# Kernel tuning notes

Hardware: AMD Instinct MI355X
Metric: run time of the kernel (lower is better)

The kernel has to match this reference:

```python
import jax, jax.numpy as jnp
import numpy as np

B, S, N = 16, 64, 4096
D = 64            # input_dim*seq_len == output_dim*graph_dim
FEAT = 64
E = 32768
HEADS = (3, 3, 1)
NEG_SLOPE = 0.2   # PyG GATConv default negative_slope


def _lin_init(key, fi, fo):
    k1, k2 = jax.random.split(key)
    s = 1.0 / np.sqrt(fi)
    return (jax.random.uniform(k1, (fi, fo), jnp.float32, -s, s),
            jax.random.uniform(k2, (fo,), jnp.float32, -s, s))


def setup_inputs() -> dict:
    key = jax.random.key(0)
    ks = jax.random.split(key, 32)
    inp = {}
    inp["inputs"] = jax.random.normal(ks[0], (B, S, N, 1), jnp.float32)
    inp["edge_index"] = jax.random.randint(ks[1], (2, E), 0, N, dtype=jnp.int32)
    inp["W_seq"], inp["b_seq"] = _lin_init(ks[2], D, D)
    inp["src_embed"] = jax.random.normal(ks[3], (N, FEAT), jnp.float32) * 0.1
    inp["tgt_embed"] = jax.random.normal(ks[4], (FEAT, N), jnp.float32) * 0.1
    for i, H in enumerate(HEADS):
        s = 1.0 / np.sqrt(D)
        inp[f"Wg{i}"] = jax.random.uniform(ks[5 + 5 * i], (D, H * D), jnp.float32, -s, s)
        inp[f"asrc{i}"] = jax.random.normal(ks[6 + 5 * i], (H, D), jnp.float32) * 0.1
        inp[f"adst{i}"] = jax.random.normal(ks[7 + 5 * i], (H, D), jnp.float32) * 0.1
        inp[f"bg{i}"] = jnp.zeros((D,), jnp.float32)
        inp[f"Wl{i}"], inp[f"bl{i}"] = _lin_init(ks[8 + 5 * i], D, D)
    inp["Wo"], inp["bo"] = _lin_init(ks[25], D, D)
    return inp


def _gat(x, src, dst, W, a_src, a_dst, b):
    # PyG GATConv, concat=False (mean over heads). x: [B,N,D] -> [B,N,D]
    H, C = a_src.shape
    xp = jnp.einsum('bnd,dhc->bnhc', x, W.reshape(D, H, C))       # [B,N,H,C]
    al_s = jnp.einsum('bnhc,hc->bnh', xp, a_src)
    al_d = jnp.einsum('bnhc,hc->bnh', xp, a_dst)
    e = jax.nn.leaky_relu(al_s[:, src] + al_d[:, dst], NEG_SLOPE)  # [B,Et,H]

    def per_graph(e_b, xj_b):
        m = jax.ops.segment_max(e_b, dst, num_segments=N)          # [N,H]
        w = jnp.exp(e_b - m[dst])
        z = jax.ops.segment_sum(w, dst, num_segments=N)
        alpha = w / z[dst]                                         # softmax per dst node
        return jax.ops.segment_sum(xj_b * alpha[..., None], dst, num_segments=N)

    out = jax.vmap(per_graph)(e, xp[:, src])                       # [B,N,H,C]
    return out.mean(axis=2) + b


def _forward(inputs, edge_index, W_seq, b_seq, src_embed, tgt_embed,
             Wg0, asrc0, adst0, bg0, Wl0, bl0,
             Wg1, asrc1, adst1, bg1, Wl1, bl1,
             Wg2, asrc2, adst2, bg2, Wl2, bl2, Wo, bo):
    loop = jnp.arange(N, dtype=edge_index.dtype)
    src = jnp.concatenate([edge_index[0], loop])   # PyG add_self_loops=True
    dst = jnp.concatenate([edge_index[1], loop])
    h = inputs.transpose(0, 2, 3, 1).reshape(B * N, D)
    h = h @ W_seq + b_seq + h                       # seq_linear residual
    A = jax.nn.softmax(jax.nn.relu(src_embed @ tgt_embed), axis=1)  # learned adjacency [N,N]
    gat_p = [(Wg0, asrc0, adst0, bg0), (Wg1, asrc1, adst1, bg1), (Wg2, asrc2, adst2, bg2)]
    lin_p = [(Wl0, bl0), (Wl1, bl1), (Wl2, bl2)]
    for i in range(3):
        hb = h.reshape(B, N, D)
        # layer-0 GAT output is computed but unused in the original code (dead); skip it
        h_cur = _gat(hb, src, dst, *gat_p[i]).reshape(B * N, D) if i > 0 else None
        adp = jnp.einsum('mn,bnd->bmd', A, hb)      # adaptive-graph matmul (dropout in eval = identity)
        adp = (adp @ lin_p[i][0] + lin_p[i][1]).reshape(B * N, D)
        g = jax.nn.sigmoid(adp)
        if i == 0:
            origin = h @ Wo + bo
            h = jnp.tanh(h) * g + origin * (1.0 - g)
        elif i == 1:
            h = jax.nn.leaky_relu(h_cur, 0.01) * g + h * (1.0 - g)
        else:
            h = jax.nn.relu(h_cur) * g + h * (1.0 - g)
    return h.reshape(B, N, 1, D)   # [batch, node_num, output_dim, graph_dim]


def reference(inputs, edge_index, W_seq, b_seq, src_embed, tgt_embed,
              Wg0, asrc0, adst0, bg0, Wl0, bl0,
              Wg1, asrc1, adst1, bg1, Wl1, bl1,
              Wg2, asrc2, adst2, bg2, Wl2, bl2, Wo, bo):
    return _forward(inputs, edge_index, W_seq, b_seq, src_embed, tgt_embed,
                    Wg0, asrc0, adst0, bg0, Wl0, bl0,
                    Wg1, asrc1, adst1, bg1, Wl1, bl1,
                    Wg2, asrc2, adst2, bg2, Wl2, bl2, Wo, bo)
```

## Files before the change

kernel.cpp:

```cpp
#include <hip/hip_runtime.h>
#include <stdint.h>

#define NB 16
#define NN 4096
#define DD 64
#define EE 32768
#define ETOT 36864
#define ROWS 65536
#define KSPLIT 4

typedef _Float16 f16;
typedef f16   half8 __attribute__((ext_vector_type(8)));
typedef f16   f16x8 __attribute__((ext_vector_type(8)));
typedef f16   f16x4 __attribute__((ext_vector_type(4)));
typedef float f32x4 __attribute__((ext_vector_type(4)));

__device__ __forceinline__ void gload16(const f16* g, f16* l) {
  __builtin_amdgcn_global_load_lds((const __attribute__((address_space(1))) void*)g,
                                   (__attribute__((address_space(3))) void*)l, 16, 0, 0);
}

__global__ __launch_bounds__(256) void k_zero2(int* a, int* b) {
  int i = blockIdx.x * 256 + threadIdx.x;
  if (i < NN) a[i] = 0;
  else if (i < 2 * NN) b[i - NN] = 0;
}

__global__ __launch_bounds__(256) void k_count(const int* __restrict__ ei, int* __restrict__ cnt) {
  int t = blockIdx.x * 256 + threadIdx.x;
  if (t >= ETOT) return;
  int d = (t < EE) ? ei[EE + t] : (t - EE);
  atomicAdd(&cnt[d], 1);
}

__global__ __launch_bounds__(256) void k_scan(const int* __restrict__ cnt, int* __restrict__ offs) {
  __shared__ int part[256];
  int t = threadIdx.x;
  int loc[16]; int s = 0;
  #pragma unroll
  for (int i = 0; i < 16; ++i) { int v = cnt[(t << 4) + i]; loc[i] = s; s += v; }
  part[t] = s;
  __syncthreads();
  int own = s;
  for (int d = 1; d < 256; d <<= 1) {
    int u = (t >= d) ? part[t - d] : 0;
    __syncthreads();
    part[t] += u;
    __syncthreads();
  }
  int base = part[t] - own;
  #pragma unroll
  for (int i = 0; i < 16; ++i) offs[(t << 4) + i] = base + loc[i];
}

__global__ __launch_bounds__(256) void k_fill(const int* __restrict__ ei, const int* __restrict__ offs,
                                              int* __restrict__ cur, int* __restrict__ esrc) {
  int t = blockIdx.x * 256 + threadIdx.x;
  if (t >= ETOT) return;
  int s, d;
  if (t < EE) { s = ei[t]; d = ei[EE + t]; } else { s = d = t - EE; }
  int p = atomicAdd(&cur[d], 1);
  esrc[offs[d] + p] = s;
}

__global__ __launch_bounds__(256) void k_seq(const float* __restrict__ inp, const float* __restrict__ Wseq,
                                             const float* __restrict__ bseq, float* __restrict__ h) {
  __shared__ float X[64 * 68];
  int t = threadIdx.x;
  int b = blockIdx.x >> 6, n0 = (blockIdx.x & 63) << 6;
  #pragma unroll
  for (int i = 0; i < 16; ++i) {
    int idx = t + (i << 8);
    int s = idx >> 6, nl = idx & 63;
    X[nl * 68 + s] = inp[((size_t)((b << 6) + s) << 12) + n0 + nl];
  }
  __syncthreads();
  int c = t & 63, rg = t >> 6;
  float Wc[64];
  #pragma unroll
  for (int k = 0; k < 64; ++k) Wc[k] = Wseq[(k << 6) + c];
  float bc = bseq[c];
  for (int rr = 0; rr < 16; ++rr) {
    int r = (rg << 4) + rr;
    float a = bc + X[r * 68 + c];
    #pragma unroll
    for (int k4 = 0; k4 < 16; ++k4) {
      float4 x = *(const float4*)&X[r * 68 + (k4 << 2)];
      a = fmaf(x.x, Wc[4*k4+0], a); a = fmaf(x.y, Wc[4*k4+1], a);
      a = fmaf(x.z, Wc[4*k4+2], a); a = fmaf(x.w, Wc[4*k4+3], a);
    }
    h[((size_t)(b << 12) + n0 + r) * 64 + c] = a;
  }
}

__global__ __launch_bounds__(256) void k_adjmm(const f16* __restrict__ SEh, const f16* __restrict__ TEh,
                                               f16* __restrict__ A, float* __restrict__ Zpart) {
  __shared__ f16 Al[2][128 * 32];
  __shared__ f16 Bl[2][128 * 32];
  const int t = threadIdx.x, lane = t & 63, w = t >> 6;
  const int m0 = blockIdx.y << 7, j0 = blockIdx.x << 7;
  const int l15 = lane & 15, lhi = lane >> 4;
  const int wm = (w >> 1) << 6, wj = (w & 1) << 6;
  f32x4 acc[4][4] = {};
  const int c0 = (w << 6) + lane;
  const int row0 = c0 >> 2, ko0 = (c0 & 3) << 3;
  const int c1 = c0 + 256;
  const int row1 = c1 >> 2, ko1 = (c1 & 3) << 3;
  const f16* ga0 = SEh + (size_t)(m0 + row0) * 64 + ko0;
  const f16* ga1 = SEh + (size_t)(m0 + row1) * 64 + ko1;
  const f16* gb0 = TEh + (size_t)(j0 + row0) * 64 + ko0;
  const f16* gb1 = TEh + (size_t)(j0 + row1) * 64 + ko1;
  #pragma unroll
  for (int kt = 0; kt < 2; ++kt) {
    const int kof = kt << 5;
    gload16(ga0 + kof, Al[kt] + c0 * 8);
    gload16(ga1 + kof, Al[kt] + c1 * 8);
    gload16(gb0 + kof, Bl[kt] + c0 * 8);
    gload16(gb1 + kof, Bl[kt] + c1 * 8);
  }
  __syncthreads();
  #pragma unroll
  for (int kt = 0; kt < 2; ++kt) {
    half8 af[4], bf[4];
    #pragma unroll
    for (int i = 0; i < 4; ++i) {
      af[i] = *(const half8*)(Al[kt] + (wm + i * 16 + l15) * 32 + lhi * 8);
      bf[i] = *(const half8*)(Bl[kt] + (wj + i * 16 + l15) * 32 + lhi * 8);
    }
    #pragma unroll
    for (int mi = 0; mi < 4; ++mi)
      #pragma unroll
      for (int nj = 0; nj < 4; ++nj)
        acc[mi][nj] = __builtin_amdgcn_mfma_f32_16x16x32_f16(af[mi], bf[nj], acc[mi][nj], 0, 0, 0);
  }
  float rs[4][4];
  #pragma unroll
  for (int mi = 0; mi < 4; ++mi)
    #pragma unroll
    for (int r = 0; r < 4; ++r) rs[mi][r] = 0.f;
  #pragma unroll
  for (int mi = 0; mi < 4; ++mi)
    #pragma unroll
    for (int nj = 0; nj < 4; ++nj)
      #pragma unroll
      for (int r = 0; r < 4; ++r) {
        int row = m0 + wm + mi * 16 + lhi * 4 + r;
        int col = j0 + wj + nj * 16 + l15;
        float e = __expf(fmaxf(acc[mi][nj][r], 0.f));
        f16 eh = (f16)e;
        A[((size_t)row << 12) + col] = eh;
        rs[mi][r] += (float)eh;
      }
  #pragma unroll
  for (int mi = 0; mi < 4; ++mi)
    #pragma unroll
    for (int r = 0; r < 4; ++r) {
      float s = rs[mi][r];
      s += __shfl_xor(s, 1); s += __shfl_xor(s, 2);
      s += __shfl_xor(s, 4); s += __shfl_xor(s, 8);
      rs[mi][r] = s;
    }
  if (l15 == 0) {
    int p = (blockIdx.x << 1) + (w & 1);
    #pragma unroll
    for (int mi = 0; mi < 4; ++mi)
      #pragma unroll
      for (int r = 0; r < 4; ++r)
        Zpart[((size_t)p << 12) + m0 + wm + mi * 16 + lhi * 4 + r] = rs[mi][r];
  }
}

__global__ __launch_bounds__(256) void k_rowz(const float* __restrict__ Zpart, float* __restrict__ rowZ) {
  int row = blockIdx.x * 256 + threadIdx.x;
  float s = 0.f;
  #pragma unroll 8
  for (int p = 0; p < 64; ++p) s += Zpart[((size_t)p << 12) + row];
  rowZ[row] = 1.f / s;
}

#define NKT 16
__global__ __launch_bounds__(512) void k_gemm8(const f16* __restrict__ A, const f16* __restrict__ BT,
                                               f16* __restrict__ Cout) {
  extern __shared__ f16 smem[];
  const int t = threadIdx.x, lane = t & 63, wid = t >> 6;
  const int wr = wid >> 2, wc = wid & 3;
  const int l15 = lane & 15, lhi = lane >> 4;
  const int h7 = l15 & 7;
  const int wgid = blockIdx.x;
  const int nid = (wgid & 7) * 32 + (wgid >> 3);
  const int z = nid >> 6, rem = nid & 63;
  const int m0 = (rem >> 2) << 8;
  const int j0 = (rem & 3) << 8;
  const size_t kbase = (size_t)z << 10;
  f16* __restrict__ Cz = Cout + ((size_t)z << 22);

  const f16* gA[4]; int lA[4];
  #pragma unroll
  for (int i = 0; i < 4; ++i) {
    int s = t + (i << 9), row = s >> 3, sl = (s & 7) ^ (row & 7);
    gA[i] = A + (size_t)(m0 + row) * 4096 + kbase + sl * 8;
    lA[i] = s * 8;
  }
  const f16* gB[4]; int lB[4];
  #pragma unroll
  for (int i = 0; i < 4; ++i) {
    int s = t + (i << 9), row = s >> 3, sl = (s & 7) ^ (row & 7);
    gB[i] = BT + (size_t)(j0 + row) * 4096 + kbase + sl * 8;
    lB[i] = 16384 + s * 8;
  }
  #define SA(buf, kt, i) gload16(gA[i] + (kt) * 64, smem + (buf) * 32768 + lA[i])
  #define SB(buf, kt, i) gload16(gB[i] + (kt) * 64, smem + (buf) * 32768 + lB[i])

  const int rbase = wr << 7;
  const int cbase = wc << 6;
  f32x4 acc[8][4] = {};

  #pragma unroll
  for (int i = 0; i < 4; ++i) SA(0, 0, i);
  #pragma unroll
  for (int i = 0; i < 4; ++i) SB(0, 0, i);
  asm volatile("s_waitcnt vmcnt(0)" ::: "memory");
  __builtin_amdgcn_sched_barrier(0);
  __builtin_amdgcn_s_barrier();
  __builtin_amdgcn_sched_barrier(0);

  for (int kt = 0; kt < NKT; ++kt) {
    const int cur = kt & 1;
    const f16* Ab = smem + cur * 32768;
    const f16* Bb = Ab + 16384;
    const bool pf = (kt + 1 < NKT);
    {
      half8 af[8], bf[4];
      #pragma unroll
      for (int mi = 0; mi < 8; ++mi) {
        int row = rbase + mi * 16 + l15;
        af[mi] = *(const half8*)(Ab + row * 64 + (lhi ^ h7) * 8);
      }
      #pragma unroll
      for (int nj = 0; nj < 4; ++nj) {
        int row = cbase + nj * 16 + l15;
        bf[nj] = *(const half8*)(Bb + row * 64 + (lhi ^ h7) * 8);
      }
      if (pf) { SA(cur ^ 1, kt + 1, 0); SA(cur ^ 1, kt + 1, 1); SA(cur ^ 1, kt + 1, 2); SA(cur ^ 1, kt + 1, 3); }
      __builtin_amdgcn_s_setprio(1);
      #pragma unroll
      for (int mi = 0; mi < 8; ++mi)
        #pragma unroll
        for (int nj = 0; nj < 4; ++nj)
          acc[mi][nj] = __builtin_amdgcn_mfma_f32_16x16x32_f16(af[mi], bf[nj], acc[mi][nj], 0, 0, 0);
      __builtin_amdgcn_s_setprio(0);
    }
    {
      half8 af[8], bf[4];
      #pragma unroll
      for (int mi = 0; mi < 8; ++mi) {
        int row = rbase + mi * 16 + l15;
        af[mi] = *(const half8*)(Ab + row * 64 + ((4 + lhi) ^ h7) * 8);
      }
      #pragma unroll
      for (int nj = 0; nj < 4; ++nj) {
        int row = cbase + nj * 16 + l15;
        bf[nj] = *(const half8*)(Bb + row * 64 + ((4 + lhi) ^ h7) * 8);
      }
      if (pf) { SB(cur ^ 1, kt + 1, 0); SB(cur ^ 1, kt + 1, 1); SB(cur ^ 1, kt + 1, 2); SB(cur ^ 1, kt + 1, 3); }
      __builtin_amdgcn_s_setprio(1);
      #pragma unroll
      for (int mi = 0; mi < 8; ++mi)
        #pragma unroll
        for (int nj = 0; nj < 4; ++nj)
          acc[mi][nj] = __builtin_amdgcn_mfma_f32_16x16x32_f16(af[mi], bf[nj], acc[mi][nj], 0, 0, 0);
      __builtin_amdgcn_s_setprio(0);
    }
    if (pf) {
      asm volatile("s_waitcnt vmcnt(0)" ::: "memory");
      __builtin_amdgcn_sched_barrier(0);
      __builtin_amdgcn_s_barrier();
      __builtin_amdgcn_sched_barrier(0);
    }
  }
  #undef SA
  #undef SB
  #pragma unroll
  for (int mi = 0; mi < 8; ++mi)
    #pragma unroll
    for (int nj = 0; nj < 4; ++nj)
      #pragma unroll
      for (int r = 0; r < 4; ++r) {
        int row = m0 + rbase + mi * 16 + (lhi << 2) + r;
        int col = j0 + cbase + nj * 16 + l15;
        Cz[(size_t)row * 1024 + col] = (f16)acc[mi][nj][r];
      }
}

template<int H, int NP>
__device__ __forceinline__ void wprep_body(const float* __restrict__ Wg, const float* __restrict__ asrc,
                                           const float* __restrict__ adst, const float* __restrict__ Wl,
                                           f16* __restrict__ Wgh, int bid, int t) {
  const int WL0 = H * 64 + 16;
  for (int i = bid * 256 + t; i < NP * 64; i += 16 * 256) {
    int j = i >> 6, k = i & 63;
    float v;
    if (j < H * 64) {
      v = Wg[(size_t)k * (H * 64) + j];
    } else if (j < H * 64 + 2 * H) {
      int cc = j - H * 64, hh = cc >> 1;
      const float* a = ((cc & 1) ? adst : asrc) + (hh << 6);
      const float* wrow = Wg + (size_t)k * (H * 64) + (hh << 6);
      float s = 0.f;
      #pragma unroll 16
      for (int c = 0; c < 64; ++c) s = fmaf(wrow[c], a[c], s);
      v = s;
    } else if (j >= WL0 && j < WL0 + 64) {
      v = Wl[(k << 6) + (j - WL0)];
    } else v = 0.f;
    Wgh[(size_t)j * 64 + k] = (f16)v;
  }
}

__global__ __launch_bounds__(256) void k_allprep(
    const float* __restrict__ Wg1, const float* __restrict__ as1, const float* __restrict__ ad1,
    const float* __restrict__ Wl1, f16* __restrict__ Wgh1,
    const float* __restrict__ Wg2, const float* __restrict__ as2, const float* __restrict__ ad2,
    const float* __restrict__ Wl2, f16* __restrict__ Wgh2,
    const float* __restrict__ Wl0, const float* __restrict__ Wo, f16* __restrict__ W0h,
    const float* __restrict__ SE, const float* __restrict__ TE,
    f16* __restrict__ SEh, f16* __restrict__ TEh) {
  __shared__ float X[64 * 65];
  int bid = blockIdx.x, t = threadIdx.x;
  if (bid < 16) { wprep_body<3, 272>(Wg1, as1, ad1, Wl1, Wgh1, bid, t); return; }
  if (bid < 32) { wprep_body<1, 144>(Wg2, as2, ad2, Wl2, Wgh2, bid - 16, t); return; }
  if (bid < 40) {
    for (int i = (bid - 32) * 256 + t; i < 128 * 64; i += 8 * 256) {
      int j = i >> 6, k = i & 63;
      float v = (j < 64) ? Wl0[(k << 6) + j] : Wo[(k << 6) + (j - 64)];
      W0h[(size_t)j * 64 + k] = (f16)v;
    }
    return;
  }
  if (bid < 296) {
    int i = ((bid - 40) * 256 + t) * 4;
    float4 v = *(const float4*)(SE + i);
    f16 o[4] = {(f16)v.x, (f16)v.y, (f16)v.z, (f16)v.w};
    *(uint64_t*)(SEh + i) = *(uint64_t*)o;
    return;
  }
  int j0 = (bid - 296) << 6;
  #pragma unroll
  for (int i = 0; i < 16; ++i) {
    int idx = t + (i << 8);
    int k = idx >> 6, jl = idx & 63;
    X[jl * 65 + k] = TE[((size_t)k << 12) + j0 + jl];
  }
  __syncthreads();
  int jl = t >> 2, kg = t & 3;
  f16 o[16];
  #pragma unroll
  for (int i = 0; i < 16; ++i) o[i] = (f16)X[jl * 65 + (kg << 4) + i];
  f16* dst = TEh + ((size_t)(j0 + jl) << 6) + (kg << 4);
  *(uint64_t*)(dst + 0) = *(uint64_t*)(o + 0);
  *(uint64_t*)(dst + 4) = *(uint64_t*)(o + 4);
  *(uint64_t*)(dst + 8) = *(uint64_t*)(o + 8);
  *(uint64_t*)(dst + 12) = *(uint64_t*)(o + 12);
}

template<int H, int NP>
__global__ __launch_bounds__(256) void k_xpmm(const float* __restrict__ h, const f16* __restrict__ Wgh,
                                              f16* __restrict__ xp, float* __restrict__ als4,
                                              float* __restrict__ ald4, f16* __restrict__ HWlT) {
  const int WL0 = H * 64 + 16, JW0 = WL0 / 16, NT = NP / 16;
  __shared__ f16 Ah[64 * 72];
  __shared__ f16 Bh[NP * 72];
  __shared__ f16 stage[64 * 72];
  const int t = threadIdx.x, lane = t & 63, w = t >> 6;
  const size_t r0 = (size_t)blockIdx.x * 64;
  const int b = (int)(r0 >> 12), n0 = (int)(r0 & 4095);
  #pragma unroll
  for (int i = 0; i < 4; ++i) {
    int idx = t + (i << 8);
    int row = idx >> 4, k4 = (idx & 15) << 2;
    float4 v = *(const float4*)&h[(r0 + row) * 64 + k4];
    f16 o[4] = {(f16)v.x, (f16)v.y, (f16)v.z, (f16)v.w};
    *(uint64_t*)&Ah[row * 72 + k4] = *(uint64_t*)o;
  }
  for (int i = t; i < NP * 16; i += 256) {
    int row = i >> 4, k4 = (i & 15) << 2;
    *(uint64_t*)&Bh[row * 72 + k4] = *(const uint64_t*)&Wgh[(size_t)row * 64 + k4];
  }
  __syncthreads();
  const int l15 = lane & 15, lhi = lane >> 4;
  f32x4 acc[NT] = {};
  #pragma unroll
  for (int kk = 0; kk < 2; ++kk) {
    half8 af = *(const half8*)&Ah[(w * 16 + l15) * 72 + kk * 32 + lhi * 8];
    #pragma unroll
    for (int j = 0; j < NT; ++j) {
      half8 bf = *(const half8*)&Bh[(j * 16 + l15) * 72 + kk * 32 + lhi * 8];
      acc[j] = __builtin_amdgcn_mfma_f32_16x16x32_f16(af, bf, acc[j], 0, 0, 0);
    }
  }
  const int rl = w * 16 + lhi * 4;
  #pragma unroll
  for (int j = 0; j < NT; ++j) {
    int col = j * 16 + l15;
    if (j * 16 + 15 < H * 64) {
      #pragma unroll
      for (int r = 0; r < 4; ++r) {
        if (H == 3) xp[(r0 + rl + r) * 256 + ((col & 63) << 2) + (col >> 6)] = (f16)acc[j][r];
        else        xp[(r0 + rl + r) * 64 + col] = (f16)acc[j][r];
      }
    } else if (j < JW0) {
      int cc = col - H * 64;
      if (cc >= 0 && cc < 2 * H) {
        int hh = cc >> 1;
        #pragma unroll
        for (int r = 0; r < 4; ++r) {
          if (cc & 1) ald4[(r0 + rl + r) * 4 + hh] = acc[j][r];
          else        als4[(r0 + rl + r) * 4 + hh] = acc[j][r];
        }
      }
    } else {
      int e = col - WL0;
      f16 o[4] = {(f16)acc[j][0], (f16)acc[j][1], (f16)acc[j][2], (f16)acc[j][3]};
      *(uint64_t*)&stage[e * 72 + rl] = *(uint64_t*)o;
    }
  }
  __syncthreads();
  {
    int e = t >> 2, seg = (t & 3) << 4;
    float4 v0 = *(const float4*)&stage[e * 72 + seg];
    float4 v1 = *(const float4*)&stage[e * 72 + seg + 8];
    f16* dst = HWlT + (((size_t)((b << 6) + e)) << 12) + n0 + seg;
    *(float4*)dst = v0;
    *(float4*)(dst + 8) = v1;
  }
}

__global__ __launch_bounds__(256) void k_prep0(const float* __restrict__ h, const f16* __restrict__ W0h,
                                               f16* __restrict__ HWlT, f16* __restrict__ orig) {
  __shared__ f16 Ah[64 * 72];
  __shared__ f16 Bh[128 * 72];
  __shared__ f16 stage[64 * 72];
  const int t = threadIdx.x, lane = t & 63, w = t >> 6;
  const size_t r0 = (size_t)blockIdx.x * 64;
  const int b = (int)(r0 >> 12), n0 = (int)(r0 & 4095);
  #pragma unroll
  for (int i = 0; i < 4; ++i) {
    int idx = t + (i << 8);
    int row = idx >> 4, k4 = (idx & 15) << 2;
    float4 v = *(const float4*)&h[(r0 + row) * 64 + k4];
    f16 o[4] = {(f16)v.x, (f16)v.y, (f16)v.z, (f16)v.w};
    *(uint64_t*)&Ah[row * 72 + k4] = *(uint64_t*)o;
  }
  for (int i = t; i < 128 * 16; i += 256) {
    int row = i >> 4, k4 = (i & 15) << 2;
    *(uint64_t*)&Bh[row * 72 + k4] = *(const uint64_t*)&W0h[(size_t)row * 64 + k4];
  }
  __syncthreads();
  const int l15 = lane & 15, lhi = lane >> 4;
  f32x4 acc[8] = {};
  #pragma unroll
  for (int kk = 0; kk < 2; ++kk) {
    half8 af = *(const half8*)&Ah[(w * 16 + l15) * 72 + kk * 32 + lhi * 8];
    #pragma unroll
    for (int j = 0; j < 8; ++j) {
      half8 bf = *(const half8*)&Bh[(j * 16 + l15) * 72 + kk * 32 + lhi * 8];
      acc[j] = __builtin_amdgcn_mfma_f32_16x16x32_f16(af, bf, acc[j], 0, 0, 0);
    }
  }
  const int rl = w * 16 + lhi * 4;
  #pragma unroll
  for (int j = 0; j < 8; ++j) {
    int col = j * 16 + l15;
    if (j < 4) {
      f16 o[4] = {(f16)acc[j][0], (f16)acc[j][1], (f16)acc[j][2], (f16)acc[j][3]};
      *(uint64_t*)&stage[col * 72 + rl] = *(uint64_t*)o;
    } else {
      #pragma unroll
      for (int r = 0; r < 4; ++r)
        orig[(r0 + rl + r) * 64 + (col - 64)] = (f16)acc[j][r];
    }
  }
  __syncthreads();
  {
    int e = t >> 2, seg = (t & 3) << 4;
    float4 v0 = *(const float4*)&stage[e * 72 + seg];
    float4 v1 = *(const float4*)&stage[e * 72 + seg + 8];
    f16* dst = HWlT + (((size_t)((b << 6) + e)) << 12) + n0 + seg;
    *(float4*)dst = v0;
    *(float4*)(dst + 8) = v1;
  }
}

template<int H, int ACT>
__global__ __launch_bounds__(256) void k_aggc(const f16* __restrict__ xp, const float* __restrict__ als4,
                                              const float* __restrict__ ald4,
                                              const int* __restrict__ offs, const int* __restrict__ cnt,
                                              const int* __restrict__ esrc, const float* __restrict__ bg,
                                              const float* __restrict__ h, const f16* __restrict__ gp,
                                              const float* __restrict__ rowZ, const float* __restrict__ bl,
                                              float* __restrict__ hout) {
  const int WST = (H == 3) ? 4 : 1;
  __shared__ float wbuf[4][64 * WST];
  __shared__ int   sbuf[4][64];
  int t = threadIdx.x, lane = t & 63, wv = t >> 6;
  int blk = blockIdx.x;
  int b = ((blk & 7) << 1) | ((blk >> 3) & 1);
  int n = ((blk >> 4) << 2) + wv;
  size_t rbase = (size_t)b << 12;
  int o = offs[n], c = cnt[n];
  float ad0 = ald4[(rbase + n) * 4 + 0];
  float ad1 = (H == 3) ? ald4[(rbase + n) * 4 + 1] : 0.f;
  float ad2 = (H == 3) ? ald4[(rbase + n) * 4 + 2] : 0.f;
  const f16* xpb = xp + (rbase << (H == 3 ? 8 : 6));
  float z[H], acc[H];
  #pragma unroll
  for (int hh = 0; hh < H; ++hh) { z[hh] = 0.f; acc[hh] = 0.f; }
  for (int e0 = 0; e0 < c; e0 += 64) {
    int ce = min(64, c - e0);
    if (lane < ce) {
      int sl = esrc[o + e0 + lane];
      sbuf[wv][lane] = sl;
      if (H == 3) {
        float4 a4 = *(const float4*)&als4[(rbase + sl) * 4];
        float ev0 = a4.x + ad0; ev0 = ev0 > 0.f ? ev0 : 0.2f * ev0;
        float ev1 = a4.y + ad1; ev1 = ev1 > 0.f ? ev1 : 0.2f * ev1;
        float ev2 = a4.z + ad2; ev2 = ev2 > 0.f ? ev2 : 0.2f * ev2;
        float4 w4;
        w4.x = __expf(fminf(ev0, 60.f));
        w4.y = __expf(fminf(ev1, 60.f));
        w4.z = __expf(fminf(ev2, 60.f));
        w4.w = 0.f;
        *(float4*)&wbuf[wv][lane * 4] = w4;
      } else {
        float ev = als4[(rbase + sl) * 4] + ad0;
        ev = ev > 0.f ? ev : 0.2f * ev;
        wbuf[wv][lane] = __expf(fminf(ev, 60.f));
      }
    }
    #pragma unroll 4
    for (int e = 0; e < ce; ++e) {
      int s = __builtin_amdgcn_readfirstlane(sbuf[wv][e]);
      if (H == 3) {
        float4 w4 = *(const float4*)&wbuf[wv][e * 4];
        f16x4 q = *(const f16x4*)(xpb + ((size_t)s << 8) + (lane << 2));
        z[0] += w4.x; acc[0] = fmaf(w4.x, (float)q[0], acc[0]);
        z[1] += w4.y; acc[1] = fmaf(w4.y, (float)q[1], acc[1]);
        z[2] += w4.z; acc[2] = fmaf(w4.z, (float)q[2], acc[2]);
      } else {
        float wv_ = wbuf[wv][e];
        float xv = (float)xpb[((size_t)s << 6) + lane];
        z[0] += wv_; acc[0] = fmaf(wv_, xv, acc[0]);
      }
    }
  }
  float r = 0.f;
  #pragma unroll
  for (int hh = 0; hh < H; ++hh) r += acc[hh] / z[hh];
  float cv = r * (1.f / H) + bg[lane];
  size_t ga = ((size_t)n << 10) + (b << 6) + lane;
  float zi = rowZ[n];
  float gs = 0.f;
  #pragma unroll
  for (int p = 0; p < KSPLIT; ++p) gs += (float)gp[ga + (size_t)p * (4096 * 1024)];
  float g = 1.f / (1.f + __expf(-(gs * zi + bl[lane])));
  size_t ridx = ((rbase + n) << 6) + lane;
  float hv = h[ridx];
  float act = ACT ? fmaxf(cv, 0.f) : (cv > 0.f ? cv : 0.01f * cv);
  hout[ridx] = act * g + hv * (1.f - g);
}

__global__ __launch_bounds__(256) void k_comb0e(const float* __restrict__ h, const f16* __restrict__ gp,
                                                const float* __restrict__ rowZ, const f16* __restrict__ orig,
                                                const float* __restrict__ bl, const float* __restrict__ bo,
                                                float* __restrict__ hout) {
  for (size_t i4 = (size_t)blockIdx.x * 256 + threadIdx.x; i4 < (size_t)ROWS * 16; i4 += (size_t)2048 * 256) {
    size_t i = i4 * 4;
    int d = (int)(i & 63), n = (int)((i >> 6) & 4095), b = (int)(i >> 18);
    size_t ga = ((size_t)n << 10) + (b << 6) + d;
    float zi = rowZ[n];
    float gs[4] = {0.f, 0.f, 0.f, 0.f};
    #pragma unroll
    for (int p = 0; p < KSPLIT; ++p) {
      f16x4 gq = *(const f16x4*)&gp[ga + (size_t)p * (4096 * 1024)];
      gs[0] += (float)gq[0]; gs[1] += (float)gq[1]; gs[2] += (float)gq[2]; gs[3] += (float)gq[3];
    }
    f16x4 og = *(const f16x4*)&orig[i];
    float4 hv = *(const float4*)&h[i];
    float4 o;
    float* op = &o.x;
    const float* hp = &hv.x;
    #pragma unroll
    for (int r = 0; r < 4; ++r) {
      float g = 1.f / (1.f + __expf(-(gs[r] * zi + bl[d + r])));
      float orv = (float)og[r] + bo[d + r];
      op[r] = tanhf(hp[r]) * g + orv * (1.f - g);
    }
    *(float4*)&hout[i] = o;
  }
}

extern "C" void kernel_launch(void* const* d_in, const int* in_sizes, int n_in,
                              void* d_out, int out_size, void* d_ws, size_t ws_size,
                              hipStream_t stream) {
  (void)in_sizes; (void)n_in; (void)out_size; (void)ws_size;
  const float* inp  = (const float*)d_in[0];
  const int*   ei   = (const int*)d_in[1];
  const float* Wseq = (const float*)d_in[2];
  const float* bseq = (const float*)d_in[3];
  const float* SE   = (const float*)d_in[4];
  const float* TE   = (const float*)d_in[5];
  const float* Wg[3]   = {(const float*)d_in[6],  (const float*)d_in[12], (const float*)d_in[18]};
  const float* asrc[3] = {(const float*)d_in[7],  (const float*)d_in[13], (const float*)d_in[19]};
  const float* adst[3] = {(const float*)d_in[8],  (const float*)d_in[14], (const float*)d_in[20]};
  const float* bgp[3]  = {(const float*)d_in[9],  (const float*)d_in[15], (const float*)d_in[21]};
  const float* Wl[3]   = {(const float*)d_in[10], (const float*)d_in[16], (const float*)d_in[22]};
  const float* bl[3]   = {(const float*)d_in[11], (const float*)d_in[17], (const float*)d_in[23]};
  const float* Wo = (const float*)d_in[24];
  const float* bo = (const float*)d_in[25];
  float* out = (float*)d_out;

  uint8_t* ws = (uint8_t*)d_ws;
  size_t o = 0;
  auto nxt = [&](size_t sz) { void* p = ws + o; o += (sz + 255) & ~(size_t)255; return p; };
  f16*   Af   = (f16*)  nxt((size_t)NN * NN * sizeof(f16));
  f16*   HWlT = (f16*)  nxt((size_t)1024 * NN * sizeof(f16));
  float* h    = (float*)nxt((size_t)ROWS * 64 * 4);
  f16*   gp   = (f16*)  nxt((size_t)KSPLIT * NN * 1024 * sizeof(f16));
  f16*   xp   = (f16*)  nxt((size_t)ROWS * 256 * sizeof(f16));
  f16*   orig = (f16*)  nxt((size_t)ROWS * 64 * sizeof(f16));
  float* als4 = (float*)nxt((size_t)ROWS * 4 * 4);
  float* ald4 = (float*)nxt((size_t)ROWS * 4 * 4);
  float* rowZ = (float*)nxt((size_t)NN * 4);
  float* Zpart= (float*)nxt((size_t)64 * NN * 4);
  f16*   SEh  = (f16*)  nxt((size_t)NN * 64 * sizeof(f16));
  f16*   TEh  = (f16*)  nxt((size_t)NN * 64 * sizeof(f16));
  f16*   Wgh1 = (f16*)  nxt((size_t)288 * 64 * sizeof(f16));
  f16*   Wgh2 = (f16*)  nxt((size_t)144 * 64 * sizeof(f16));
  f16*   W0h  = (f16*)  nxt((size_t)128 * 64 * sizeof(f16));
  int*   cnt  = (int*)  nxt((size_t)NN * 4);
  int*   curp = (int*)  nxt((size_t)NN * 4);
  int*   offs = (int*)  nxt((size_t)NN * 4);
  int*   esrc = (int*)  nxt((size_t)ETOT * 4);

  static bool attr_set = false;
  if (!attr_set) {
    hipFuncSetAttribute((const void*)k_gemm8, hipFuncAttributeMaxDynamicSharedMemorySize, 131072);
    attr_set = true;
  }

  dim3 blk(256);
  k_zero2<<<32, blk, 0, stream>>>(cnt, curp);
  k_count<<<144, blk, 0, stream>>>(ei, cnt);
  k_scan<<<1, blk, 0, stream>>>(cnt, offs);
  k_fill<<<144, blk, 0, stream>>>(ei, offs, curp, esrc);
  k_allprep<<<360, blk, 0, stream>>>(Wg[1], asrc[1], adst[1], Wl[1], Wgh1,
                                     Wg[2], asrc[2], adst[2], Wl[2], Wgh2,
                                     Wl[0], Wo, W0h, SE, TE, SEh, TEh);
  k_seq<<<1024, blk, 0, stream>>>(inp, Wseq, bseq, h);
  k_adjmm<<<dim3(32, 32), blk, 0, stream>>>(SEh, TEh, Af, Zpart);
  k_rowz<<<16, blk, 0, stream>>>(Zpart, rowZ);
  k_prep0<<<1024, blk, 0, stream>>>(h, W0h, HWlT, orig);
  k_gemm8<<<256, 512, 131072, stream>>>(Af, HWlT, gp);
  k_comb0e<<<2048, blk, 0, stream>>>(h, gp, rowZ, orig, bl[0], bo, h);
  k_xpmm<3, 272><<<1024, blk, 0, stream>>>(h, Wgh1, xp, als4, ald4, HWlT);
  k_gemm8<<<256, 512, 131072, stream>>>(Af, HWlT, gp);
  k_aggc<3, 0><<<16384, blk, 0, stream>>>(xp, als4, ald4, offs, cnt, esrc, bgp[1], h, gp, rowZ, bl[1], h);
  k_xpmm<1, 144><<<1024, blk, 0, stream>>>(h, Wgh2, xp, als4, ald4, HWlT);
  k_gemm8<<<256, 512, 131072, stream>>>(Af, HWlT, gp);
  k_aggc<1, 1><<<16384, blk, 0, stream>>>(xp, als4, ald4, offs, cnt, esrc, bgp[2], h, gp, rowZ, bl[2], out);
}
```

Measured before the change: 308.4 us.

## Precompute GAT edge weights in separate kernel and aggregate two batches per wave

Moves the per-edge leaky-relu/exp attention weight computation out of the aggregation kernel into a new k_wts kernel, with a CSR-ordered dst array added to k_fill. k_aggc now handles two batch elements per wave, sharing the edge-index loads and halving the grid. The aim is to amortise index loads and expose more memory-level parallelism in the gather. The cost is an extra kernel launch per layer and a written-then-reread weights buffer. readfirstlane on the source index is also dropped, which may move that address from a scalar to a vector register.

Measured after the change: 282.6 us (median of 2 runs). 1.09x faster.

```diff
diff --git a/kernel.cpp b/kernel.cpp
--- a/kernel.cpp
+++ b/kernel.cpp
@@ -54,13 +54,15 @@
 }
 
 __global__ __launch_bounds__(256) void k_fill(const int* __restrict__ ei, const int* __restrict__ offs,
-                                              int* __restrict__ cur, int* __restrict__ esrc) {
+                                              int* __restrict__ cur, int* __restrict__ esrc,
+                                              int* __restrict__ edst) {
   int t = blockIdx.x * 256 + threadIdx.x;
   if (t >= ETOT) return;
   int s, d;
   if (t < EE) { s = ei[t]; d = ei[EE + t]; } else { s = d = t - EE; }
   int p = atomicAdd(&cur[d], 1);
   esrc[offs[d] + p] = s;
+  edst[offs[d] + p] = d;
 }
 
 __global__ __launch_bounds__(256) void k_seq(const float* __restrict__ inp, const float* __restrict__ Wseq,
@@ -491,82 +493,110 @@
   }
 }
 
+template<int H>
+__global__ __launch_bounds__(256) void k_wts(const float* __restrict__ als4, const float* __restrict__ ald4,
+                                             const int* __restrict__ esrc, const int* __restrict__ edst,
+                                             float* __restrict__ wts) {
+  const int WST = (H == 3) ? 4 : 1;
+  int t = threadIdx.x, lane = t & 63, w = t >> 6;
+  int gw = blockIdx.x * 4 + w;
+  int b = gw & 15;
+  int p = ((gw >> 4) << 6) + lane;
+  size_t rbase = (size_t)b << 12;
+  int s = esrc[p], n = edst[p];
+  float4 a4 = *(const float4*)&als4[(rbase + s) * 4];
+  float4 d4 = *(const float4*)&ald4[(rbase + n) * 4];
+  const float* ap = &a4.x;
+  const float* dp = &d4.x;
+  float* dst = wts + ((size_t)b * ETOT + p) * WST;
+  #pragma unroll
+  for (int h = 0; h < H; ++h) {
+    float ev = ap[h] + dp[h];
+    ev = ev > 0.f ? ev : 0.2f * ev;
+    dst[h] = __expf(fminf(ev, 60.f));
+  }
+}
+
 template<int H, int ACT>
-__global__ __launch_bounds__(256) void k_aggc(const f16* __restrict__ xp, const float* __restrict__ als4,
-                                              const float* __restrict__ ald4,
+__global__ __launch_bounds__(256) void k_aggc(const f16* __restrict__ xp, const float* __restrict__ wts,
                                               const int* __restrict__ offs, const int* __restrict__ cnt,
                                               const int* __restrict__ esrc, const float* __restrict__ bg,
                                               const float* __restrict__ h, const f16* __restrict__ gp,
                                               const float* __restrict__ rowZ, const float* __restrict__ bl,
                                               float* __restrict__ hout) {
   const int WST = (H == 3) ? 4 : 1;
-  __shared__ float wbuf[4][64 * WST];
+  __shared__ float wbuf[4][64 * WST * 2];
   __shared__ int   sbuf[4][64];
   int t = threadIdx.x, lane = t & 63, wv = t >> 6;
   int blk = blockIdx.x;
-  int b = ((blk & 7) << 1) | ((blk >> 3) & 1);
-  int n = ((blk >> 4) << 2) + wv;
-  size_t rbase = (size_t)b << 12;
+  int b0 = (blk & 7) << 1, b1 = b0 | 1;
+  int n = ((blk >> 3) << 2) + wv;
+  size_t rb0 = (size_t)b0 << 12, rb1 = (size_t)b1 << 12;
   int o = offs[n], c = cnt[n];
-  float ad0 = ald4[(rbase + n) * 4 + 0];
-  float ad1 = (H == 3) ? ald4[(rbase + n) * 4 + 1] : 0.f;
-  float ad2 = (H == 3) ? ald4[(rbase + n) * 4 + 2] : 0.f;
-  const f16* xpb = xp + (rbase << (H == 3 ? 8 : 6));
-  float z[H], acc[H];
-  #pragma unroll
-  for (int hh = 0; hh < H; ++hh) { z[hh] = 0.f; acc[hh] = 0.f; }
+  const float* ws0 = wts + ((size_t)b0 * ETOT + o) * WST;
+  const float* ws1 = wts + ((size_t)b1 * ETOT + o) * WST;
+  const int xsh = (H == 3) ? 8 : 6;
+  const f16* xp0 = xp + (rb0 << xsh);
+  const f16* xp1 = xp + (rb1 << xsh);
+  float z0[H], a0[H], z1[H], a1[H];
+  #pragma unroll
+  for (int hh = 0; hh < H; ++hh) { z0[hh] = 0.f; a0[hh] = 0.f; z1[hh] = 0.f; a1[hh] = 0.f; }
   for (int e0 = 0; e0 < c; e0 += 64) {
     int ce = min(64, c - e0);
     if (lane < ce) {
-      int sl = esrc[o + e0 + lane];
-      sbuf[wv][lane] = sl;
+      sbuf[wv][lane] = esrc[o + e0 + lane];
       if (H == 3) {
-        float4 a4 = *(const float4*)&als4[(rbase + sl) * 4];
-        float ev0 = a4.x + ad0; ev0 = ev0 > 0.f ? ev0 : 0.2f * ev0;
-        float ev1 = a4.y + ad1; ev1 = ev1 > 0.f ? ev1 : 0.2f * ev1;
-        float ev2 = a4.z + ad2; ev2 = ev2 > 0.f ? ev2 : 0.2f * ev2;
-        float4 w4;
-        w4.x = __expf(fminf(ev0, 60.f));
-        w4.y = __expf(fminf(ev1, 60.f));
-        w4.z = __expf(fminf(ev2, 60.f));
-        w4.w = 0.f;
-        *(float4*)&wbuf[wv][lane * 4] = w4;
+        *(float4*)&wbuf[wv][lane * 8]     = *(const float4*)&ws0[(size_t)(e0 + lane) * 4];
+        *(float4*)&wbuf[wv][lane * 8 + 4] = *(const float4*)&ws1[(size_t)(e0 + lane) * 4];
       } else {
-        float ev = als4[(rbase + sl) * 4] + ad0;
-        ev = ev > 0.f ? ev : 0.2f * ev;
-        wbuf[wv][lane] = __expf(fminf(ev, 60.f));
+        wbuf[wv][lane * 2]     = ws0[e0 + lane];
+        wbuf[wv][lane * 2 + 1] = ws1[e0 + lane];
       }
     }
     #pragma unroll 4
     for (int e = 0; e < ce; ++e) {
-      int s = __builtin_amdgcn_readfirstlane(sbuf[wv][e]);
+      int s = sbuf[wv][e];
       if (H == 3) {
-        float4 w4 = *(const float4*)&wbuf[wv][e * 4];
-        f16x4 q = *(const f16x4*)(xpb + ((size_t)s << 8) + (lane << 2));
-        z[0] += w4.x; acc[0] = fmaf(w4.x, (float)q[0], acc[0]);
-        z[1] += w4.y; acc[1] = fmaf(w4.y, (float)q[1], acc[1]);
-        z[2] += w4.z; acc[2] = fmaf(w4.z, (float)q[2], acc[2]);
+        float4 w40 = *(const float4*)&wbuf[wv][e * 8];
+        float4 w41 = *(const float4*)&wbuf[wv][e * 8 + 4];
+        f16x4 q0 = *(const f16x4*)(xp0 + ((size_t)s << 8) + (lane << 2));
+        f16x4 q1 = *(const f16x4*)(xp1 + ((size_t)s << 8) + (lane << 2));
+        z0[0] += w40.x; a0[0] = fmaf(w40.x, (float)q0[0], a0[0]);
+        z0[1] += w40.y; a0[1] = fmaf(w40.y, (float)q0[1], a0[1]);
+        z0[2] += w40.z; a0[2] = fmaf(w40.z, (float)q0[2], a0[2]);
+        z1[0] += w41.x; a1[0] = fmaf(w41.x, (float)q1[0], a1[0]);
+        z1[1] += w41.y; a1[1] = fmaf(w41.y, (float)q1[1], a1[1]);
+        z1[2] += w41.z; a1[2] = fmaf(w41.z, (float)q1[2], a1[2]);
       } else {
-        float wv_ = wbuf[wv][e];
-        float xv = (float)xpb[((size_t)s << 6) + lane];
-        z[0] += wv_; acc[0] = fmaf(wv_, xv, acc[0]);
-      }
-    }
-  }
-  float r = 0.f;
-  #pragma unroll
-  for (int hh = 0; hh < H; ++hh) r += acc[hh] / z[hh];
-  float cv = r * (1.f / H) + bg[lane];
-  size_t ga = ((size_t)n << 10) + (b << 6) + lane;
-  float zi = rowZ[n];
-  float gs = 0.f;
-  #pragma unroll
-  for (int p = 0; p < KSPLIT; ++p) gs += (float)gp[ga + (size_t)p * (4096 * 1024)];
-  float g = 1.f / (1.f + __expf(-(gs * zi + bl[lane])));
-  size_t ridx = ((rbase + n) << 6) + lane;
-  float hv = h[ridx];
-  float act = ACT ? fmaxf(cv, 0.f) : (cv > 0.f ? cv : 0.01f * cv);
-  hout[ridx] = act * g + hv * (1.f - g);
+        float w0 = wbuf[wv][e * 2], w1 = wbuf[wv][e * 2 + 1];
+        float x0 = (float)xp0[((size_t)s << 6) + lane];
+        float x1 = (float)xp1[((size_t)s << 6) + lane];
+        z0[0] += w0; a0[0] = fmaf(w0, x0, a0[0]);
+        z1[0] += w1; a1[0] = fmaf(w1, x1, a1[0]);
+      }
+    }
+  }
+  float bgl = bg[lane], bll = bl[lane], zi = rowZ[n];
+  #pragma unroll
+  for (int pb = 0; pb < 2; ++pb) {
+    int b = pb ? b1 : b0;
+    size_t rb = pb ? rb1 : rb0;
+    float* zz = pb ? z1 : z0;
+    float* aa = pb ? a1 : a0;
+    float r = 0.f;
+    #pragma unroll
+    for (int hh = 0; hh < H; ++hh) r += aa[hh] / zz[hh];
+    float cv = r * (1.f / H) + bgl;
+    size_t ga = ((size_t)n << 10) + (b << 6) + lane;
+    float gs = 0.f;
+    #pragma unroll
+    for (int p = 0; p < KSPLIT; ++p) gs += (float)gp[ga + (size_t)p * (4096 * 1024)];
+    float g = 1.f / (1.f + __expf(-(gs * zi + bll)));
+    size_t ridx = ((rb + n) << 6) + lane;
+    float hv = h[ridx];
+    float act = ACT ? fmaxf(cv, 0.f) : (cv > 0.f ? cv : 0.01f * cv);
+    hout[ridx] = act * g + hv * (1.f - g);
+  }
 }
 
 __global__ __launch_bounds__(256) void k_comb0e(const float* __restrict__ h, const f16* __restrict__ gp,
@@ -637,10 +667,12 @@
   f16*   Wgh1 = (f16*)  nxt((size_t)288 * 64 * sizeof(f16));
   f16*   Wgh2 = (f16*)  nxt((size_t)144 * 64 * sizeof(f16));
   f16*   W0h  = (f16*)  nxt((size_t)128 * 64 * sizeof(f16));
+  float* wts  = (float*)nxt((size_t)NB * ETOT * 4 * 4);
   int*   cnt  = (int*)  nxt((size_t)NN * 4);
   int*   curp = (int*)  nxt((size_t)NN * 4);
   int*   offs = (int*)  nxt((size_t)NN * 4);
   int*   esrc = (int*)  nxt((size_t)ETOT * 4);
+  int*   edst = (int*)  nxt((size_t)ETOT * 4);
 
   static bool attr_set = false;
   if (!attr_set) {
@@ -652,7 +684,7 @@
   k_zero2<<<32, blk, 0, stream>>>(cnt, curp);
   k_count<<<144, blk, 0, stream>>>(ei, cnt);
   k_scan<<<1, blk, 0, stream>>>(cnt, offs);
-  k_fill<<<144, blk, 0, stream>>>(ei, offs, curp, esrc);
+  k_fill<<<144, blk, 0, stream>>>(ei, offs, curp, esrc, edst);
   k_allprep<<<360, blk, 0, stream>>>(Wg[1], asrc[1], adst[1], Wl[1], Wgh1,
                                      Wg[2], asrc[2], adst[2], Wl[2], Wgh2,
                                      Wl[0], Wo, W0h, SE, TE, SEh, TEh);
@@ -663,9 +695,11 @@
   k_gemm8<<<256, 512, 131072, stream>>>(Af, HWlT, gp);
   k_comb0e<<<2048, blk, 0, stream>>>(h, gp, rowZ, orig, bl[0], bo, h);
   k_xpmm<3, 272><<<1024, blk, 0, stream>>>(h, Wgh1, xp, als4, ald4, HWlT);
+  k_wts<3><<<2304, blk, 0, stream>>>(als4, ald4, esrc, edst, wts);
   k_gemm8<<<256, 512, 131072, stream>>>(Af, HWlT, gp);
-  k_aggc<3, 0><<<16384, blk, 0, stream>>>(xp, als4, ald4, offs, cnt, esrc, bgp[1], h, gp, rowZ, bl[1], h);
+  k_aggc<3, 0><<<8192, blk, 0, stream>>>(xp, wts, offs, cnt, esrc, bgp[1], h, gp, rowZ, bl[1], h);
   k_xpmm<1, 144><<<1024, blk, 0, stream>>>(h, Wgh2, xp, als4, ald4, HWlT);
+  k_wts<1><<<2304, blk, 0, stream>>>(als4, ald4, esrc, edst, wts);
   k_gemm8<<<256, 512, 131072, stream>>>(Af, HWlT, gp);
-  k_aggc<1, 1><<<16384, blk, 0, stream>>>(xp, als4, ald4, offs, cnt, esrc, bgp[2], h, gp, rowZ, bl[2], out);
-}
+  k_aggc<1, 1><<<8192, blk, 0, stream>>>(xp, wts, offs, cnt, esrc, bgp[2], h, gp, rowZ, bl[2], out);
+}
```
